# Kernel tuning notes

Hardware: AMD Instinct MI355X
Metric: run time of the kernel (lower is better)

The kernel has to match this reference:

```python
import jax, jax.numpy as jnp
import numpy as np

EMB = 256
T = 32          # block_size (hardcoded causal mask length)
HEAD = 128      # total head_size
NH = 8          # n_heads
DH = HEAD // NH # 16 per-head size
B = 4096
EPS = 1e-5


def _ln(x, g, b):
    mu = jnp.mean(x, -1, keepdims=True)
    var = jnp.var(x, -1, keepdims=True)
    return (x - mu) * jax.lax.rsqrt(var + EPS) * g + b


def setup_inputs() -> dict:
    key = jax.random.key(0)
    ks = jax.random.split(key, 12)
    s_in = 1.0 / np.sqrt(EMB)
    s_h = 1.0 / np.sqrt(HEAD)
    s_ff = 1.0 / np.sqrt(4 * EMB)
    return {
        "X": jax.random.normal(ks[0], (B, T, EMB), jnp.float32),
        "ln_g": jnp.ones((EMB,), jnp.float32),
        "ln_b": jnp.zeros((EMB,), jnp.float32),
        # per-head Q/K/V projections packed: [EMB, HEAD] == concat of NH [EMB, DH] heads
        "Wq": jax.random.uniform(ks[1], (EMB, HEAD), jnp.float32, -s_in, s_in),
        "bq": jax.random.uniform(ks[2], (HEAD,), jnp.float32, -s_in, s_in),
        "Wk": jax.random.uniform(ks[3], (EMB, HEAD), jnp.float32, -s_in, s_in),
        "bk": jax.random.uniform(ks[4], (HEAD,), jnp.float32, -s_in, s_in),
        "Wv": jax.random.uniform(ks[5], (EMB, HEAD), jnp.float32, -s_in, s_in),
        "bv": jax.random.uniform(ks[6], (HEAD,), jnp.float32, -s_in, s_in),
        "Wo": jax.random.uniform(ks[7], (HEAD, EMB), jnp.float32, -s_h, s_h),
        "bo": jax.random.uniform(ks[8], (EMB,), jnp.float32, -s_h, s_h),
        "W1": jax.random.uniform(ks[9], (EMB, 4 * EMB), jnp.float32, -s_in, s_in),
        "b1": jax.random.uniform(ks[10], (4 * EMB,), jnp.float32, -s_in, s_in),
        "W2": jax.random.uniform(ks[11], (4 * EMB, EMB), jnp.float32, -s_ff, s_ff),
        "b2": jax.random.uniform(jax.random.fold_in(key, 99), (EMB,), jnp.float32, -s_ff, s_ff),
    }


def reference(X, ln_g, ln_b, Wq, bq, Wk, bk, Wv, bv, Wo, bo, W1, b1, W2, b2):
    h = _ln(X, ln_g, ln_b)                              # [B,T,E]
    # packed QKV, split into heads: [B,T,NH,DH]
    Q = (h @ Wq + bq).reshape(B, T, NH, DH)
    K = (h @ Wk + bk).reshape(B, T, NH, DH)
    V = (h @ Wv + bv).reshape(B, T, NH, DH)
    scores = jnp.einsum("bqhd,bkhd->bhqk", Q, K)        # [B,NH,T,T]
    mask = jnp.tril(jnp.ones((T, T), bool))
    # original: masked_fill(-inf) then divide by sqrt(dh); -inf unchanged
    scores = jnp.where(mask, scores / np.sqrt(DH), -jnp.inf)
    attn = jax.nn.softmax(scores, -1)
    ctx = jnp.einsum("bhqk,bkhd->bqhd", attn, V).reshape(B, T, HEAD)
    X = ctx @ Wo + bo + X                               # residual 1
    h2 = _ln(X, ln_g, ln_b)                             # shared LN params
    out = jax.nn.relu(h2 @ W1 + b1) @ W2 + b2 + X       # residual 2
    return out
```

## Files before the change

kernel.cpp:

```cpp
#include <hip/hip_runtime.h>
#include <math.h>

typedef __attribute__((ext_vector_type(8))) __bf16 bf16x8;
typedef __attribute__((ext_vector_type(8))) unsigned short u16x8;
typedef __attribute__((ext_vector_type(4))) unsigned short u16x4;
typedef __attribute__((ext_vector_type(4))) float f32x4;

namespace {
constexpr int EMB = 256;
constexpr int HD  = 128;
constexpr int FF  = 1024;
constexpr float EPSV = 1e-5f;

constexpr int WS_QKV = 0;
constexpr int WS_O   = 98304;
constexpr int WS_1   = 131072;
constexpr int WS_2   = 393216;

__device__ __forceinline__ unsigned short f32_to_bf16(float f) {
    return __builtin_bit_cast(unsigned short, (__bf16)f);
}
__device__ __forceinline__ float bf16_to_f32(unsigned short h) {
    return __builtin_bit_cast(float, ((unsigned int)h) << 16);
}
__device__ __forceinline__ f32x4 mfma16(u16x8 a, u16x8 b, f32x4 c) {
    return __builtin_amdgcn_mfma_f32_16x16x32_bf16(
        __builtin_bit_cast(bf16x8, a), __builtin_bit_cast(bf16x8, b), c, 0, 0, 0);
}
__device__ __forceinline__ int swzB(int row) { return (row & 7) << 4; }

__device__ __forceinline__ u16x8 ldsA256(const unsigned short* base, int row, int k0) {
    int byte = (row * 256 + k0 * 2) ^ swzB(row);
    return *(const u16x8*)((const char*)base + byte);
}
__device__ __forceinline__ u16x8 ldsA512(const unsigned short* base, int row, int k0) {
    int byte = (row * 512 + k0 * 2) ^ swzB(row);
    return *(const u16x8*)((const char*)base + byte);
}
__device__ __forceinline__ u16x8 ldgF(const unsigned short* base, int frag, int lane) {
    return *(const u16x8*)(base + ((size_t)frag * 64 + lane) * 8);
}
}

__global__ __launch_bounds__(256) void wconv(
    const float* __restrict__ Wq, const float* __restrict__ Wk, const float* __restrict__ Wv,
    const float* __restrict__ Wo, const float* __restrict__ W1, const float* __restrict__ W2,
    unsigned short* __restrict__ ws) {
    int e = blockIdx.x * 256 + threadIdx.x;
    int j, lane, kk, nt, n, k;
    float v;
    if (e < WS_O) {
        int t = e; j = t & 7; lane = (t >> 3) & 63; int r2 = t >> 9;
        kk = r2 & 7; nt = r2 >> 3;
        n = nt * 16 + (lane & 15); k = kk * 32 + (lane >> 4) * 8 + j;
        const float* W = (n < 128) ? Wq : ((n < 256) ? Wk : Wv);
        v = W[k * HD + (n & 127)];
    } else if (e < WS_1) {
        int t = e - WS_O; j = t & 7; lane = (t >> 3) & 63; int r2 = t >> 9;
        kk = r2 & 3; nt = r2 >> 2;
        n = nt * 16 + (lane & 15); k = kk * 32 + (lane >> 4) * 8 + j;
        v = Wo[k * EMB + n];
    } else if (e < WS_2) {
        int t = e - WS_1; j = t & 7; lane = (t >> 3) & 63; int r2 = t >> 9;
        kk = r2 & 7; nt = r2 >> 3;
        n = nt * 16 + (lane & 15); k = kk * 32 + (lane >> 4) * 8 + j;
        v = W1[k * FF + n];
    } else {
        int t = e - WS_2; j = t & 7; lane = (t >> 3) & 63; int r2 = t >> 9;
        kk = r2 & 31; nt = r2 >> 5;
        n = nt * 16 + (lane & 15); k = kk * 32 + (lane >> 4) * 8 + j;
        v = W2[k * EMB + n];
    }
    ws[e] = f32_to_bf16(v);
}

__global__ __launch_bounds__(256, 2) void attn_part(
    const float* __restrict__ X, const float* __restrict__ ln_g, const float* __restrict__ ln_b,
    const float* __restrict__ bq, const float* __restrict__ bk, const float* __restrict__ bv,
    const float* __restrict__ bo, const unsigned short* __restrict__ ws,
    float* __restrict__ x1out) {
    __shared__ __attribute__((aligned(16))) char smem[40960];
    unsigned short* hb = (unsigned short*)smem;
    unsigned short* Qb = (unsigned short*)(smem + 16384);
    char* Kc           = smem + 24576;
    char* Vc           = smem + 32768;

    const unsigned short* WTqkv = ws + WS_QKV;
    const unsigned short* WTo   = ws + WS_O;

    const int tid  = threadIdx.x;
    const int wv   = tid >> 6;
    const int mh   = wv & 1;
    const int nh   = wv >> 1;
    const int lane = tid & 63;
    const int lr   = lane & 15;
    const int lh   = lane >> 4;
    const int row0 = blockIdx.x * 32;
    const f32x4 Z  = {0.f, 0.f, 0.f, 0.f};

    {
        const int r = tid >> 3, sub = tid & 7;
        const float* xr = X + (size_t)(row0 + r) * EMB;
        float4 vv[8];
        float s = 0.f, ss = 0.f;
        #pragma unroll
        for (int j = 0; j < 8; ++j) {
            float4 v = *(const float4*)&xr[sub * 4 + j * 32];
            vv[j] = v;
            s  += (v.x + v.y) + (v.z + v.w);
            ss += (v.x * v.x + v.y * v.y) + (v.z * v.z + v.w * v.w);
        }
        #pragma unroll
        for (int w = 1; w < 8; w <<= 1) { s += __shfl_xor(s, w, 64); ss += __shfl_xor(ss, w, 64); }
        float mu  = s * (1.f / EMB);
        float inv = rsqrtf(fmaxf(ss * (1.f / EMB) - mu * mu, 0.f) + EPSV);
        #pragma unroll
        for (int j = 0; j < 8; ++j) {
            int c = sub * 4 + j * 32;
            float4 v = vv[j];
            float4 g4 = *(const float4*)&ln_g[c];
            float4 b4 = *(const float4*)&ln_b[c];
            u16x4 pk;
            pk[0] = f32_to_bf16((v.x - mu) * inv * g4.x + b4.x);
            pk[1] = f32_to_bf16((v.y - mu) * inv * g4.y + b4.y);
            pk[2] = f32_to_bf16((v.z - mu) * inv * g4.z + b4.z);
            pk[3] = f32_to_bf16((v.w - mu) * inv * g4.w + b4.w);
            *(u16x4*)((char*)hb + ((r * 512 + c * 2) ^ swzB(r))) = pk;
        }
    }
    __syncthreads();

    {
        u16x8 afr[8];
        #pragma unroll
        for (int kk = 0; kk < 8; ++kk)
            afr[kk] = ldsA512(hb, mh * 16 + lr, kk * 32 + lh * 8);
        u16x8 bfrA[8], bfrB[8];
        #pragma unroll
        for (int kk = 0; kk < 8; ++kk) bfrA[kk] = ldgF(WTqkv, (nh * 12) * 8 + kk, lane);
        #pragma unroll 1
        for (int ii = 0; ii < 6; ++ii) {
            int nt0 = nh * 12 + ii * 2;
            #pragma unroll
            for (int kk = 0; kk < 8; ++kk) bfrB[kk] = ldgF(WTqkv, (nt0 + 1) * 8 + kk, lane);
            {
                f32x4 e = Z, o = Z;
                #pragma unroll
                for (int kk = 0; kk < 8; kk += 2) {
                    e = mfma16(afr[kk], bfrA[kk], e);
                    o = mfma16(afr[kk + 1], bfrA[kk + 1], o);
                }
                f32x4 a = e + o;
                int gcol = nt0 * 16 + lr;
                int mat = gcol >> 7, c = gcol & 127;
                const float* bias = (mat == 0) ? bq : ((mat == 1) ? bk : bv);
                float bc = bias[c];
                char* regbase = smem + 16384 + mat * 8192;
                #pragma unroll
                for (int reg = 0; reg < 4; ++reg) {
                    int r0 = mh * 16 + lh * 4 + reg;
                    *(unsigned short*)(regbase + ((r0 * 256 + c * 2) ^ swzB(r0))) =
                        f32_to_bf16(a[reg] + bc);
                }
            }
            if (ii < 5) {
                #pragma unroll
                for (int kk = 0; kk < 8; ++kk) bfrA[kk] = ldgF(WTqkv, (nt0 + 2) * 8 + kk, lane);
            }
            {
                f32x4 e = Z, o = Z;
                #pragma unroll
                for (int kk = 0; kk < 8; kk += 2) {
                    e = mfma16(afr[kk], bfrB[kk], e);
                    o = mfma16(afr[kk + 1], bfrB[kk + 1], o);
                }
                f32x4 a = e + o;
                int gcol = (nt0 + 1) * 16 + lr;
                int mat = gcol >> 7, c = gcol & 127;
                const float* bias = (mat == 0) ? bq : ((mat == 1) ? bk : bv);
                float bc = bias[c];
                char* regbase = smem + 16384 + mat * 8192;
                #pragma unroll
                for (int reg = 0; reg < 4; ++reg) {
                    int r0 = mh * 16 + lh * 4 + reg;
                    *(unsigned short*)(regbase + ((r0 * 256 + c * 2) ^ swzB(r0))) =
                        f32_to_bf16(a[reg] + bc);
                }
            }
        }
    }
    __syncthreads();

    {
        const int hd = tid >> 5, q = tid & 31;
        int by0 = (q * 256 + hd * 32) ^ swzB(q);
        int by1 = (q * 256 + hd * 32 + 16) ^ swzB(q);
        float qreg[16];
        {
            u16x8 a = *(const u16x8*)((const char*)Qb + by0);
            u16x8 b_ = *(const u16x8*)((const char*)Qb + by1);
            #pragma unroll
            for (int j = 0; j < 8; ++j) { qreg[j] = bf16_to_f32(a[j]); qreg[8 + j] = bf16_to_f32(b_[j]); }
        }
        unsigned int ps[16];
        float mmax = -1e30f;
        #pragma unroll
        for (int k = 0; k < 32; ++k) {
            int kb0 = (k * 256 + hd * 32) ^ swzB(k);
            int kb1 = (k * 256 + hd * 32 + 16) ^ swzB(k);
            u16x8 a = *(const u16x8*)(Kc + kb0);
            u16x8 b_ = *(const u16x8*)(Kc + kb1);
            float s_ = 0.f;
            #pragma unroll
            for (int j = 0; j < 8; ++j)
                s_ += qreg[j] * bf16_to_f32(a[j]) + qreg[8 + j] * bf16_to_f32(b_[j]);
            s_ *= 0.25f;
            unsigned short us = f32_to_bf16(s_);
            if ((k & 1) == 0) ps[k >> 1] = (unsigned int)us;
            else              ps[k >> 1] |= ((unsigned int)us) << 16;
            if (k <= q) mmax = fmaxf(mmax, bf16_to_f32(us));
        }
        float den = 0.f;
        float ctx[16];
        #pragma unroll
        for (int j = 0; j < 16; ++j) ctx[j] = 0.f;
        #pragma unroll
        for (int k = 0; k < 32; ++k) {
            unsigned short us = (unsigned short)((k & 1) ? (ps[k >> 1] >> 16) : (ps[k >> 1] & 0xFFFFu));
            float s_ = bf16_to_f32(us);
            float e = (k <= q) ? __expf(s_ - mmax) : 0.f;
            den += e;
            int kb0 = (k * 256 + hd * 32) ^ swzB(k);
            int kb1 = (k * 256 + hd * 32 + 16) ^ swzB(k);
            u16x8 va = *(const u16x8*)(Vc + kb0);
            u16x8 vb = *(const u16x8*)(Vc + kb1);
            #pragma unroll
            for (int j = 0; j < 8; ++j) { ctx[j] += e * bf16_to_f32(va[j]); ctx[8 + j] += e * bf16_to_f32(vb[j]); }
        }
        float rd = 1.f / den;
        u16x8 o0, o1;
        #pragma unroll
        for (int j = 0; j < 8; ++j) { o0[j] = f32_to_bf16(ctx[j] * rd); o1[j] = f32_to_bf16(ctx[8 + j] * rd); }
        *(u16x8*)((char*)Qb + by0) = o0;
        *(u16x8*)((char*)Qb + by1) = o1;
    }
    __syncthreads();

    {
        u16x8 afr[4];
        #pragma unroll
        for (int kk = 0; kk < 4; ++kk)
            afr[kk] = ldsA256(Qb, mh * 16 + lr, kk * 32 + lh * 8);
        u16x8 bfrA[4], bfrB[4];
        #pragma unroll
        for (int kk = 0; kk < 4; ++kk) bfrA[kk] = ldgF(WTo, (nh * 8) * 4 + kk, lane);
        #pragma unroll 1
        for (int ii = 0; ii < 4; ++ii) {
            int nt0 = nh * 8 + ii * 2;
            #pragma unroll
            for (int kk = 0; kk < 4; ++kk) bfrB[kk] = ldgF(WTo, (nt0 + 1) * 4 + kk, lane);
            {
                int col = nt0 * 16 + lr;
                float bc = bo[col];
                f32x4 e = Z, o = Z;
                e = mfma16(afr[0], bfrA[0], e);
                o = mfma16(afr[1], bfrA[1], o);
                e = mfma16(afr[2], bfrA[2], e);
                o = mfma16(afr[3], bfrA[3], o);
                f32x4 a = e + o;
                #pragma unroll
                for (int reg = 0; reg < 4; ++reg) {
                    int r0 = mh * 16 + lh * 4 + reg;
                    size_t gi = (size_t)(row0 + r0) * EMB + col;
                    x1out[gi] = a[reg] + bc + X[gi];
                }
            }
            if (ii < 3) {
                #pragma unroll
                for (int kk = 0; kk < 4; ++kk) bfrA[kk] = ldgF(WTo, (nt0 + 2) * 4 + kk, lane);
            }
            {
                int col = (nt0 + 1) * 16 + lr;
                float bc = bo[col];
                f32x4 e = Z, o = Z;
                e = mfma16(afr[0], bfrB[0], e);
                o = mfma16(afr[1], bfrB[1], o);
                e = mfma16(afr[2], bfrB[2], e);
                o = mfma16(afr[3], bfrB[3], o);
                f32x4 a = e + o;
                #pragma unroll
                for (int reg = 0; reg < 4; ++reg) {
                    int r0 = mh * 16 + lh * 4 + reg;
                    size_t gi = (size_t)(row0 + r0) * EMB + col;
                    x1out[gi] = a[reg] + bc + X[gi];
                }
            }
        }
    }
}

__global__ __launch_bounds__(512, 1) void ffn_part(
    const float* __restrict__ ln_g, const float* __restrict__ ln_b,
    const float* __restrict__ b1, const float* __restrict__ b2,
    const unsigned short* __restrict__ ws, float* __restrict__ io) {
    __shared__ __attribute__((aligned(16))) char smem[49152];
    unsigned short* h2  = (unsigned short*)smem;
    unsigned short* fch = (unsigned short*)(smem + 32768);

    const unsigned short* WT1 = ws + WS_1;
    const unsigned short* WT2 = ws + WS_2;

    const int tid  = threadIdx.x;
    const int wv   = tid >> 6;
    const int lane = tid & 63;
    const int lr   = lane & 15;
    const int lh   = lane >> 4;
    const int row0 = blockIdx.x * 64;
    const f32x4 Z  = {0.f, 0.f, 0.f, 0.f};

    {
        const int r = tid >> 3, sub = tid & 7;
        const float* xr = io + (size_t)(row0 + r) * EMB;
        float4 vv[8];
        float s = 0.f, ss = 0.f;
        #pragma unroll
        for (int j = 0; j < 8; ++j) {
            float4 v = *(const float4*)&xr[sub * 4 + j * 32];
            vv[j] = v;
            s  += (v.x + v.y) + (v.z + v.w);
            ss += (v.x * v.x + v.y * v.y) + (v.z * v.z + v.w * v.w);
        }
        #pragma unroll
        for (int w = 1; w < 8; w <<= 1) { s += __shfl_xor(s, w, 64); ss += __shfl_xor(ss, w, 64); }
        float mu  = s * (1.f / EMB);
        float inv = rsqrtf(fmaxf(ss * (1.f / EMB) - mu * mu, 0.f) + EPSV);
        #pragma unroll
        for (int j = 0; j < 8; ++j) {
            int c = sub * 4 + j * 32;
            float4 v = vv[j];
            float4 g4 = *(const float4*)&ln_g[c];
            float4 b4 = *(const float4*)&ln_b[c];
            u16x4 pk;
            pk[0] = f32_to_bf16((v.x - mu) * inv * g4.x + b4.x);
            pk[1] = f32_to_bf16((v.y - mu) * inv * g4.y + b4.y);
            pk[2] = f32_to_bf16((v.z - mu) * inv * g4.z + b4.z);
            pk[3] = f32_to_bf16((v.w - mu) * inv * g4.w + b4.w);
            *(u16x4*)((char*)h2 + ((r * 512 + c * 2) ^ swzB(r))) = pk;
        }
    }
    __syncthreads();

    {
        f32x4 acc2[4][2];
        #pragma unroll
        for (int mt = 0; mt < 4; ++mt) { acc2[mt][0] = Z; acc2[mt][1] = Z; }

        #pragma unroll 1
        for (int ch = 0; ch < 8; ++ch) {
            {
                int fn = ch * 8 + wv;
                u16x8 bAll[8];
                #pragma unroll
                for (int kk = 0; kk < 8; ++kk) bAll[kk] = ldgF(WT1, fn * 8 + kk, lane);
                float bc = b1[fn * 16 + lr];
                int cc = wv * 16 + lr;
                #pragma unroll 1
                for (int mt = 0; mt < 4; ++mt) {
                    u16x8 afr[8];
                    #pragma unroll
                    for (int kk = 0; kk < 8; ++kk)
                        afr[kk] = ldsA512(h2, mt * 16 + lr, kk * 32 + lh * 8);
                    f32x4 e = Z, o = Z;
                    #pragma unroll
                    for (int kk = 0; kk < 8; kk += 2) {
                        e = mfma16(afr[kk], bAll[kk], e);
                        o = mfma16(afr[kk + 1], bAll[kk + 1], o);
                    }
                    f32x4 a = e + o;
                    #pragma unroll
                    for (int reg = 0; reg < 4; ++reg) {
                        int r0 = mt * 16 + lh * 4 + reg;
                        *(unsigned short*)((char*)fch + ((r0 * 256 + cc * 2) ^ swzB(r0))) =
                            f32_to_bf16(fmaxf(a[reg] + bc, 0.f));
                    }
                }
            }
            __syncthreads();
            #pragma unroll
            for (int i = 0; i < 2; ++i) {
                u16x8 b2f[4];
                #pragma unroll
                for (int kk = 0; kk < 4; ++kk)
                    b2f[kk] = ldgF(WT2, (wv * 2 + i) * 32 + ch * 4 + kk, lane);
                #pragma unroll
                for (int mt = 0; mt < 4; ++mt) {
                    u16x8 afr2[4];
                    #pragma unroll
                    for (int kk = 0; kk < 4; ++kk)
                        afr2[kk] = ldsA256(fch, mt * 16 + lr, kk * 32 + lh * 8);
                    f32x4 t = acc2[mt][i];
                    t = mfma16(afr2[0], b2f[0], t);
                    t = mfma16(afr2[1], b2f[1], t);
                    t = mfma16(afr2[2], b2f[2], t);
                    t = mfma16(afr2[3], b2f[3], t);
                    acc2[mt][i] = t;
                }
            }
            __syncthreads();
        }
        #pragma unroll
        for (int i = 0; i < 2; ++i) {
            int col = (wv * 2 + i) * 16 + lr;
            float bc = b2[col];
            #pragma unroll
            for (int mt = 0; mt < 4; ++mt) {
                #pragma unroll
                for (int reg = 0; reg < 4; ++reg) {
                    int r0 = mt * 16 + lh * 4 + reg;
                    size_t gi = (size_t)(row0 + r0) * EMB + col;
                    io[gi] = acc2[mt][i][reg] + bc + io[gi];
                }
            }
        }
    }
}

extern "C" void kernel_launch(void* const* d_in, const int* in_sizes, int n_in,
                              void* d_out, int out_size, void* d_ws, size_t ws_size,
                              hipStream_t stream) {
    const float* X    = (const float*)d_in[0];
    const float* ln_g = (const float*)d_in[1];
    const float* ln_b = (const float*)d_in[2];
    const float* Wq   = (const float*)d_in[3];
    const float* bq   = (const float*)d_in[4];
    const float* Wk   = (const float*)d_in[5];
    const float* bk   = (const float*)d_in[6];
    const float* Wv   = (const float*)d_in[7];
    const float* bv   = (const float*)d_in[8];
    const float* Wo   = (const float*)d_in[9];
    const float* bo   = (const float*)d_in[10];
    const float* W1   = (const float*)d_in[11];
    const float* b1   = (const float*)d_in[12];
    const float* W2   = (const float*)d_in[13];
    const float* b2   = (const float*)d_in[14];
    unsigned short* ws = (unsigned short*)d_ws;
    float* O = (float*)d_out;

    wconv<<<2560, 256, 0, stream>>>(Wq, Wk, Wv, Wo, W1, W2, ws);
    attn_part<<<4096, 256, 0, stream>>>(X, ln_g, ln_b, bq, bk, bv, bo, ws, O);
    ffn_part<<<2048, 512, 0, stream>>>(ln_g, ln_b, b1, b2, ws, O);
}
```

Measured before the change: 345.6 us.

## Store Q/K/V in fp32 shared memory and pair M-tiles in FFN1

The QKV projection now writes fp32 Q, K and V into a 64 KB shared buffer instead of bf16, so the attention loop reads float4 values directly and skips bf16 unpacking. The attention output now goes into the freed h buffer. Separately, the FFN1 loop processes two M-tiles per iteration, interleaving their MFMAs to expose more instruction-level parallelism. Shared memory per block grows from 40 KB to 64 KB, which may limit how many blocks fit per CU under launch_bounds(256,2), and attention LDS traffic doubles.

```diff
diff --git a/kernel.cpp b/kernel.cpp
--- a/kernel.cpp
+++ b/kernel.cpp
@@ -79,11 +79,11 @@
     const float* __restrict__ bq, const float* __restrict__ bk, const float* __restrict__ bv,
     const float* __restrict__ bo, const unsigned short* __restrict__ ws,
     float* __restrict__ x1out) {
-    __shared__ __attribute__((aligned(16))) char smem[40960];
+    __shared__ __attribute__((aligned(16))) char smem[65536];
     unsigned short* hb = (unsigned short*)smem;
-    unsigned short* Qb = (unsigned short*)(smem + 16384);
-    char* Kc           = smem + 24576;
-    char* Vc           = smem + 32768;
+    char* Qf           = smem + 16384;
+    char* Kf           = smem + 32768;
+    char* Vf           = smem + 49152;
 
     const unsigned short* WTqkv = ws + WS_QKV;
     const unsigned short* WTo   = ws + WS_O;
@@ -155,12 +155,11 @@
                 int mat = gcol >> 7, c = gcol & 127;
                 const float* bias = (mat == 0) ? bq : ((mat == 1) ? bk : bv);
                 float bc = bias[c];
-                char* regbase = smem + 16384 + mat * 8192;
+                char* regbase = smem + 16384 + mat * 16384;
                 #pragma unroll
                 for (int reg = 0; reg < 4; ++reg) {
                     int r0 = mh * 16 + lh * 4 + reg;
-                    *(unsigned short*)(regbase + ((r0 * 256 + c * 2) ^ swzB(r0))) =
-                        f32_to_bf16(a[reg] + bc);
+                    *(float*)(regbase + ((r0 * 512 + c * 4) ^ swzB(r0))) = a[reg] + bc;
                 }
             }
             if (ii < 5) {
@@ -179,12 +178,11 @@
                 int mat = gcol >> 7, c = gcol & 127;
                 const float* bias = (mat == 0) ? bq : ((mat == 1) ? bk : bv);
                 float bc = bias[c];
-                char* regbase = smem + 16384 + mat * 8192;
+                char* regbase = smem + 16384 + mat * 16384;
                 #pragma unroll
                 for (int reg = 0; reg < 4; ++reg) {
                     int r0 = mh * 16 + lh * 4 + reg;
-                    *(unsigned short*)(regbase + ((r0 * 256 + c * 2) ^ swzB(r0))) =
-                        f32_to_bf16(a[reg] + bc);
+                    *(float*)(regbase + ((r0 * 512 + c * 4) ^ swzB(r0))) = a[reg] + bc;
                 }
             }
         }
@@ -193,27 +191,24 @@
 
     {
         const int hd = tid >> 5, q = tid & 31;
-        int by0 = (q * 256 + hd * 32) ^ swzB(q);
-        int by1 = (q * 256 + hd * 32 + 16) ^ swzB(q);
         float qreg[16];
-        {
-            u16x8 a = *(const u16x8*)((const char*)Qb + by0);
-            u16x8 b_ = *(const u16x8*)((const char*)Qb + by1);
-            #pragma unroll
-            for (int j = 0; j < 8; ++j) { qreg[j] = bf16_to_f32(a[j]); qreg[8 + j] = bf16_to_f32(b_[j]); }
+        #pragma unroll
+        for (int t = 0; t < 4; ++t) {
+            float4 v = *(const float4*)(Qf + ((q * 512 + hd * 64 + t * 16) ^ swzB(q)));
+            qreg[t * 4 + 0] = v.x; qreg[t * 4 + 1] = v.y;
+            qreg[t * 4 + 2] = v.z; qreg[t * 4 + 3] = v.w;
         }
         unsigned int ps[16];
         float mmax = -1e30f;
         #pragma unroll
         for (int k = 0; k < 32; ++k) {
-            int kb0 = (k * 256 + hd * 32) ^ swzB(k);
-            int kb1 = (k * 256 + hd * 32 + 16) ^ swzB(k);
-            u16x8 a = *(const u16x8*)(Kc + kb0);
-            u16x8 b_ = *(const u16x8*)(Kc + kb1);
             float s_ = 0.f;
             #pragma unroll
-            for (int j = 0; j < 8; ++j)
-                s_ += qreg[j] * bf16_to_f32(a[j]) + qreg[8 + j] * bf16_to_f32(b_[j]);
+            for (int t = 0; t < 4; ++t) {
+                float4 v = *(const float4*)(Kf + ((k * 512 + hd * 64 + t * 16) ^ swzB(k)));
+                s_ += qreg[t * 4 + 0] * v.x + qreg[t * 4 + 1] * v.y
+                    + qreg[t * 4 + 2] * v.z + qreg[t * 4 + 3] * v.w;
+            }
             s_ *= 0.25f;
             unsigned short us = f32_to_bf16(s_);
             if ((k & 1) == 0) ps[k >> 1] = (unsigned int)us;
@@ -227,22 +222,23 @@
         #pragma unroll
         for (int k = 0; k < 32; ++k) {
             unsigned short us = (unsigned short)((k & 1) ? (ps[k >> 1] >> 16) : (ps[k >> 1] & 0xFFFFu));
-            float s_ = bf16_to_f32(us);
-            float e = (k <= q) ? __expf(s_ - mmax) : 0.f;
+            float e = (k <= q) ? __expf(bf16_to_f32(us) - mmax) : 0.f;
             den += e;
-            int kb0 = (k * 256 + hd * 32) ^ swzB(k);
-            int kb1 = (k * 256 + hd * 32 + 16) ^ swzB(k);
-            u16x8 va = *(const u16x8*)(Vc + kb0);
-            u16x8 vb = *(const u16x8*)(Vc + kb1);
-            #pragma unroll
-            for (int j = 0; j < 8; ++j) { ctx[j] += e * bf16_to_f32(va[j]); ctx[8 + j] += e * bf16_to_f32(vb[j]); }
+            #pragma unroll
+            for (int t = 0; t < 4; ++t) {
+                float4 v = *(const float4*)(Vf + ((k * 512 + hd * 64 + t * 16) ^ swzB(k)));
+                ctx[t * 4 + 0] += e * v.x; ctx[t * 4 + 1] += e * v.y;
+                ctx[t * 4 + 2] += e * v.z; ctx[t * 4 + 3] += e * v.w;
+            }
         }
         float rd = 1.f / den;
         u16x8 o0, o1;
         #pragma unroll
         for (int j = 0; j < 8; ++j) { o0[j] = f32_to_bf16(ctx[j] * rd); o1[j] = f32_to_bf16(ctx[8 + j] * rd); }
-        *(u16x8*)((char*)Qb + by0) = o0;
-        *(u16x8*)((char*)Qb + by1) = o1;
+        int by0 = (q * 256 + hd * 32) ^ swzB(q);
+        int by1 = (q * 256 + hd * 32 + 16) ^ swzB(q);
+        *(u16x8*)((char*)hb + by0) = o0;
+        *(u16x8*)((char*)hb + by1) = o1;
     }
     __syncthreads();
 
@@ -250,7 +246,7 @@
         u16x8 afr[4];
         #pragma unroll
         for (int kk = 0; kk < 4; ++kk)
-            afr[kk] = ldsA256(Qb, mh * 16 + lr, kk * 32 + lh * 8);
+            afr[kk] = ldsA256(hb, mh * 16 + lr, kk * 32 + lh * 8);
         u16x8 bfrA[4], bfrB[4];
         #pragma unroll
         for (int kk = 0; kk < 4; ++kk) bfrA[kk] = ldgF(WTo, (nh * 8) * 4 + kk, lane);
@@ -365,23 +361,31 @@
                 float bc = b1[fn * 16 + lr];
                 int cc = wv * 16 + lr;
                 #pragma unroll 1
-                for (int mt = 0; mt < 4; ++mt) {
-                    u16x8 afr[8];
+                for (int mtp = 0; mtp < 4; mtp += 2) {
+                    u16x8 afr0[8], afr1[8];
                     #pragma unroll
                     for (int kk = 0; kk < 8; ++kk)
-                        afr[kk] = ldsA512(h2, mt * 16 + lr, kk * 32 + lh * 8);
-                    f32x4 e = Z, o = Z;
+                        afr0[kk] = ldsA512(h2, (mtp + 0) * 16 + lr, kk * 32 + lh * 8);
+                    #pragma unroll
+                    for (int kk = 0; kk < 8; ++kk)
+                        afr1[kk] = ldsA512(h2, (mtp + 1) * 16 + lr, kk * 32 + lh * 8);
+                    f32x4 e0 = Z, o0 = Z, e1 = Z, o1 = Z;
                     #pragma unroll
                     for (int kk = 0; kk < 8; kk += 2) {
-                        e = mfma16(afr[kk], bAll[kk], e);
-                        o = mfma16(afr[kk + 1], bAll[kk + 1], o);
+                        e0 = mfma16(afr0[kk], bAll[kk], e0);
+                        e1 = mfma16(afr1[kk], bAll[kk], e1);
+                        o0 = mfma16(afr0[kk + 1], bAll[kk + 1], o0);
+                        o1 = mfma16(afr1[kk + 1], bAll[kk + 1], o1);
                     }
-                    f32x4 a = e + o;
+                    f32x4 a0 = e0 + o0, a1 = e1 + o1;
                     #pragma unroll
                     for (int reg = 0; reg < 4; ++reg) {
-                        int r0 = mt * 16 + lh * 4 + reg;
+                        int r0 = (mtp + 0) * 16 + lh * 4 + reg;
                         *(unsigned short*)((char*)fch + ((r0 * 256 + cc * 2) ^ swzB(r0))) =
-                            f32_to_bf16(fmaxf(a[reg] + bc, 0.f));
+                            f32_to_bf16(fmaxf(a0[reg] + bc, 0.f));
+                        int r1 = (mtp + 1) * 16 + lh * 4 + reg;
+                        *(unsigned short*)((char*)fch + ((r1 * 256 + cc * 2) ^ swzB(r1))) =
+                            f32_to_bf16(fmaxf(a1[reg] + bc, 0.f));
                     }
                 }
             }
```

After: 408.1 us. +18.1%, slower.

## Shrink FFN block to 32 rows and 4 waves, doubling per-wave output tiles

Applied to the files above, without the earlier changes.

The FFN kernel now handles 32 rows per block with 256 threads instead of 64 rows with 512 threads, and the grid doubles to 4096 blocks. Each wave computes two hidden-column chunks in the first GEMM and four output-column tiles in the second, and its A fragments are loaded once per chunk and reused across those tiles. Shared memory is halved and launch bounds allow two blocks per CU, aiming for more resident blocks and overlap. The cost is that each row block reads the full W1/W2 weights from global memory, so total weight traffic doubles.

```diff
diff --git a/kernel.cpp b/kernel.cpp
--- a/kernel.cpp
+++ b/kernel.cpp
@@ -299,13 +299,13 @@
     }
 }
 
-__global__ __launch_bounds__(512, 1) void ffn_part(
+__global__ __launch_bounds__(256, 2) void ffn_part(
     const float* __restrict__ ln_g, const float* __restrict__ ln_b,
     const float* __restrict__ b1, const float* __restrict__ b2,
     const unsigned short* __restrict__ ws, float* __restrict__ io) {
-    __shared__ __attribute__((aligned(16))) char smem[49152];
+    __shared__ __attribute__((aligned(16))) char smem[24576];
     unsigned short* h2  = (unsigned short*)smem;
-    unsigned short* fch = (unsigned short*)(smem + 32768);
+    unsigned short* fch = (unsigned short*)(smem + 16384);
 
     const unsigned short* WT1 = ws + WS_1;
     const unsigned short* WT2 = ws + WS_2;
@@ -315,7 +315,7 @@
     const int lane = tid & 63;
     const int lr   = lane & 15;
     const int lh   = lane >> 4;
-    const int row0 = blockIdx.x * 64;
+    const int row0 = blockIdx.x * 32;
     const f32x4 Z  = {0.f, 0.f, 0.f, 0.f};
 
     {
@@ -351,21 +351,24 @@
     __syncthreads();
 
     {
-        f32x4 acc2[4][2];
-        #pragma unroll
-        for (int mt = 0; mt < 4; ++mt) { acc2[mt][0] = Z; acc2[mt][1] = Z; }
+        f32x4 acc2[2][4];
+        #pragma unroll
+        for (int mt = 0; mt < 2; ++mt)
+            #pragma unroll
+            for (int i = 0; i < 4; ++i) acc2[mt][i] = Z;
 
         #pragma unroll 1
         for (int ch = 0; ch < 8; ++ch) {
-            {
-                int fn = ch * 8 + wv;
+            #pragma unroll
+            for (int f = 0; f < 2; ++f) {
+                int fn = ch * 8 + wv * 2 + f;
                 u16x8 bAll[8];
                 #pragma unroll
                 for (int kk = 0; kk < 8; ++kk) bAll[kk] = ldgF(WT1, fn * 8 + kk, lane);
                 float bc = b1[fn * 16 + lr];
-                int cc = wv * 16 + lr;
+                int cc = (wv * 2 + f) * 16 + lr;
                 #pragma unroll 1
-                for (int mt = 0; mt < 4; ++mt) {
+                for (int mt = 0; mt < 2; ++mt) {
                     u16x8 afr[8];
                     #pragma unroll
                     for (int kk = 0; kk < 8; ++kk)
@@ -386,34 +389,41 @@
                 }
             }
             __syncthreads();
-            #pragma unroll
-            for (int i = 0; i < 2; ++i) {
-                u16x8 b2f[4];
-                #pragma unroll
-                for (int kk = 0; kk < 4; ++kk)
-                    b2f[kk] = ldgF(WT2, (wv * 2 + i) * 32 + ch * 4 + kk, lane);
-                #pragma unroll
-                for (int mt = 0; mt < 4; ++mt) {
-                    u16x8 afr2[4];
+            {
+                u16x8 afr2[2][4];
+                #pragma unroll
+                for (int mt = 0; mt < 2; ++mt)
                     #pragma unroll
                     for (int kk = 0; kk < 4; ++kk)
-                        afr2[kk] = ldsA256(fch, mt * 16 + lr, kk * 32 + lh * 8);
-                    f32x4 t = acc2[mt][i];
-                    t = mfma16(afr2[0], b2f[0], t);
-                    t = mfma16(afr2[1], b2f[1], t);
-                    t = mfma16(afr2[2], b2f[2], t);
-                    t = mfma16(afr2[3], b2f[3], t);
-                    acc2[mt][i] = t;
+                        afr2[mt][kk] = ldsA256(fch, mt * 16 + lr, kk * 32 + lh * 8);
+                #pragma unroll 1
+                for (int i = 0; i < 4; ++i) {
+                    u16x8 b2f[4];
+                    #pragma unroll
+                    for (int kk = 0; kk < 4; ++kk)
+                        b2f[kk] = ldgF(WT2, (wv * 4 + i) * 32 + ch * 4 + kk, lane);
+                    f32x4 t0 = acc2[0][i];
+                    t0 = mfma16(afr2[0][0], b2f[0], t0);
+                    t0 = mfma16(afr2[0][1], b2f[1], t0);
+                    t0 = mfma16(afr2[0][2], b2f[2], t0);
+                    t0 = mfma16(afr2[0][3], b2f[3], t0);
+                    acc2[0][i] = t0;
+                    f32x4 t1 = acc2[1][i];
+                    t1 = mfma16(afr2[1][0], b2f[0], t1);
+                    t1 = mfma16(afr2[1][1], b2f[1], t1);
+                    t1 = mfma16(afr2[1][2], b2f[2], t1);
+                    t1 = mfma16(afr2[1][3], b2f[3], t1);
+                    acc2[1][i] = t1;
                 }
             }
             __syncthreads();
         }
         #pragma unroll
-        for (int i = 0; i < 2; ++i) {
-            int col = (wv * 2 + i) * 16 + lr;
+        for (int i = 0; i < 4; ++i) {
+            int col = (wv * 4 + i) * 16 + lr;
             float bc = b2[col];
             #pragma unroll
-            for (int mt = 0; mt < 4; ++mt) {
+            for (int mt = 0; mt < 2; ++mt) {
                 #pragma unroll
                 for (int reg = 0; reg < 4; ++reg) {
                     int r0 = mt * 16 + lh * 4 + reg;
@@ -448,5 +458,5 @@
 
     wconv<<<2560, 256, 0, stream>>>(Wq, Wk, Wv, Wo, W1, W2, ws);
     attn_part<<<4096, 256, 0, stream>>>(X, ln_g, ln_b, bq, bk, bv, bo, ws, O);
-    ffn_part<<<2048, 512, 0, stream>>>(ln_g, ln_b, b1, b2, ws, O);
-}
+    ffn_part<<<4096, 256, 0, stream>>>(ln_g, ln_b, b1, b2, ws, O);
+}
```

Result: slower. 380.2 us (+10.0%).
